# Kernel optimization log

Hardware: AMD Instinct MI355X
Metric: run time of the kernel (lower is better)

Reference implementation:

```python
import jax, jax.numpy as jnp
import numpy as np

B, S, D = 8, 512, 768
H = 12          # attention heads
E = 14          # routed experts
K = 4           # top-k experts per sequence
HID = D * 2     # expert mlp hidden (mlp_ratio=2)
SH = D * 2 * 2  # shared expert hidden (mlp_ratio * n_shared_experts)
EPS = 1e-5


def _ln(x, g, b):
    m = x.mean(-1, keepdims=True)
    v = ((x - m) ** 2).mean(-1, keepdims=True)
    return (x - m) / jnp.sqrt(v + EPS) * g + b


def _gelu(x):
    return jax.nn.gelu(x, approximate=False)


def setup_inputs() -> dict:
    key = jax.random.key(0)
    ks = jax.random.split(key, 12)
    p = lambda k, shape: jax.random.normal(k, shape, jnp.float32) * 0.02
    z = lambda *shape: jnp.zeros(shape, jnp.float32)
    return {
        "x": jax.random.normal(ks[0], (B, S, D), jnp.float32),
        "ln1_g": jnp.ones((D,), jnp.float32), "ln1_b": z(D),
        "qkv_w": p(ks[1], (D, 3 * D)),
        "proj_w": p(ks[2], (D, D)), "proj_b": z(D),
        "ln2_g": jnp.ones((D,), jnp.float32), "ln2_b": z(D),
        "router_w1": p(ks[3], (D, D)), "router_b1": z(D),
        "router_w2": p(ks[4], (D, E)), "router_b2": z(E),
        "exp_w1": p(ks[5], (E, D, HID)), "exp_b1": z(E, HID),
        "exp_w2": p(ks[6], (E, HID, D)), "exp_b2": z(E, D),
        "sh_w1": p(ks[7], (D, SH)), "sh_b1": z(SH),
        "sh_w2": p(ks[8], (SH, D)), "sh_b2": z(D),
    }


def _forward(x, ln1_g, ln1_b, qkv_w, proj_w, proj_b, ln2_g, ln2_b,
             router_w1, router_b1, router_w2, router_b2,
             exp_w1, exp_b1, exp_w2, exp_b2,
             sh_w1, sh_b1, sh_w2, sh_b2):
    dh = D // H
    scale = dh ** -0.5
    # --- attention branch ---
    h1 = _ln(x, ln1_g, ln1_b)
    qkv = (h1 @ qkv_w).reshape(B, S, 3, H, dh)
    q = jnp.moveaxis(qkv[:, :, 0], 2, 1)  # [B,H,S,dh]
    k = jnp.moveaxis(qkv[:, :, 1], 2, 1)
    v = jnp.moveaxis(qkv[:, :, 2], 2, 1)
    att = jax.nn.softmax(jnp.einsum('bhqd,bhkd->bhqk', q, k) * scale, axis=-1)
    ao = jnp.einsum('bhqk,bhkd->bqhd', att, v).reshape(B, S, D) @ proj_w + proj_b
    x2 = x + ao
    # --- MoE branch ---
    h = _ln(x2, ln2_g, ln2_b)
    seq_repr = h.mean(axis=1)                                   # [B,D]
    logits = _gelu(seq_repr @ router_w1 + router_b1) @ router_w2 + router_b2  # [B,E]
    probs = jax.nn.softmax(logits, axis=-1)
    tw, ti = jax.lax.top_k(probs, K)                            # [B,K]
    tw = jax.nn.softmax(tw, axis=-1)                            # re-normalize top-k
    w = (jax.nn.one_hot(ti, E, dtype=tw.dtype) * tw[..., None]).sum(1)  # [B,E]
    # dense all-expert compute; zero weight off the top-k replicates masked routing
    hid = _gelu(jnp.einsum('bsd,edh->ebsh', h, exp_w1) + exp_b1[:, None, None, :])
    eo = jnp.einsum('ebsh,ehd->ebsd', hid, exp_w2) + exp_b2[:, None, None, :]
    y = jnp.einsum('ebsd,be->bsd', eo, w)
    # shared experts
    y = y + _gelu(h @ sh_w1 + sh_b1) @ sh_w2 + sh_b2
    return x2 + y  # ls2 is Identity (init_values=None); aux_loss=0 in eval


def reference(x, ln1_g, ln1_b, qkv_w, proj_w, proj_b, ln2_g, ln2_b,
              router_w1, router_b1, router_w2, router_b2,
              exp_w1, exp_b1, exp_w2, exp_b2,
              sh_w1, sh_b1, sh_w2, sh_b2):
    return _forward(x, ln1_g, ln1_b, qkv_w, proj_w, proj_b, ln2_g, ln2_b,
                    router_w1, router_b1, router_w2, router_b2,
                    exp_w1, exp_b1, exp_w2, exp_b2,
                    sh_w1, sh_b1, sh_w2, sh_b2)
```

## Files before the change

### kernel.cpp

```cpp
#include <hip/hip_runtime.h>
#include <hip/hip_bf16.h>


typedef _Float16 f16x8 __attribute__((ext_vector_type(8)));
typedef float f32x4 __attribute__((ext_vector_type(4)));
typedef _Float16 f16;

__device__ __forceinline__ float gelu_fast(float x) {
  const float k2l2e = 2.f * 0.7978845608028654f * 1.4426950408889634f;
  float u = (x + 0.044715f * x * x * x) * k2l2e;
  float t = exp2f(u);
  return x * (1.f - 1.f / (t + 1.f));
}

__device__ __forceinline__ f32x4 mfma16(f16x8 a, f16x8 b, f32x4 c) {
  return __builtin_amdgcn_mfma_f32_16x16x32_f16(a, b, c, 0, 0, 0);
}

#define ASYNC_CP16(g, l)                                            \
  __builtin_amdgcn_global_load_lds(                                 \
      (const __attribute__((address_space(1))) void*)(g),           \
      (__attribute__((address_space(3))) void*)(l), 16, 0, 0)

__global__ __launch_bounds__(256) void ln_kernel(
    const float* __restrict__ x, const float* __restrict__ g,
    const float* __restrict__ bt, f16* __restrict__ out,
    float* __restrict__ mout, float* __restrict__ rout)
{
  const int row = blockIdx.x;
  const float* xr = x + (long)row * 768;
  const int t = threadIdx.x;
  float v0 = xr[t], v1 = xr[t + 256], v2 = xr[t + 512];
  __shared__ float sb[8];
  float s = v0 + v1 + v2;
  #pragma unroll
  for (int o = 32; o > 0; o >>= 1) s += __shfl_xor(s, o, 64);
  const int w = t >> 6;
  if ((t & 63) == 0) sb[w] = s;
  __syncthreads();
  const float mean = (sb[0] + sb[1] + sb[2] + sb[3]) * (1.0f / 768.0f);
  const float d0 = v0 - mean, d1 = v1 - mean, d2 = v2 - mean;
  float q = d0 * d0 + d1 * d1 + d2 * d2;
  #pragma unroll
  for (int o = 32; o > 0; o >>= 1) q += __shfl_xor(q, o, 64);
  if ((t & 63) == 0) sb[4 + w] = q;
  __syncthreads();
  const float var = (sb[4] + sb[5] + sb[6] + sb[7]) * (1.0f / 768.0f);
  const float rstd = rsqrtf(var + 1e-5f);
  f16* orow = out + (long)row * 768;
  orow[t]       = (f16)(d0 * rstd * g[t]       + bt[t]);
  orow[t + 256] = (f16)(d1 * rstd * g[t + 256] + bt[t + 256]);
  orow[t + 512] = (f16)(d2 * rstd * g[t + 512] + bt[t + 512]);
  if (t == 0) { mout[row] = mean; rout[row] = rstd; }
}

struct TransArgs {
  const float* src[6];
  f16* dst[6];
  int rows[6], cols[6];
  int start[7];
};

__global__ __launch_bounds__(256) void transpose_all(TransArgs ta) {
  const int bid = blockIdx.x;
  int m = 0;
  #pragma unroll
  for (int i = 1; i < 6; i++) if (bid >= ta.start[i]) m = i;
  const int rows = ta.rows[m], cols = ta.cols[m];
  const int tilesC = cols >> 5;
  const int perB = (rows >> 5) * tilesC;
  int local = bid - ta.start[m];
  const int z = local / perB; local -= z * perB;
  const int tr = local / tilesC, tc = local - tr * tilesC;
  const float* inb = ta.src[m] + (long)z * rows * cols;
  f16* outb = ta.dst[m] + (long)z * rows * cols;
  const int c0 = tc * 32, r0 = tr * 32;
  __shared__ float tile[32][33];
  const int tx = threadIdx.x & 31, ty = threadIdx.x >> 5;
  #pragma unroll
  for (int i = 0; i < 32; i += 8)
    tile[ty + i][tx] = inb[(long)(r0 + ty + i) * cols + c0 + tx];
  __syncthreads();
  #pragma unroll
  for (int i = 0; i < 32; i += 8)
    outb[(long)(c0 + ty + i) * rows + r0 + tx] = (f16)tile[tx][ty + i];
}

#define EPI_QKV     0
#define EPI_RESID   1
#define EPI_GELU    2
#define EPI_OUTBASE 3
#define EPI_GELUW   4
#define EPI_SCB     5

template <int EPI>
__global__ __launch_bounds__(256) void gemm_bt(
    const f16* __restrict__ A, int K, long strideA, int aShift,
    const f16* __restrict__ W, long strideW,
    const float* __restrict__ bias, int strideBias,
    const int* __restrict__ topkIdx,
    void* __restrict__ outv, long strideOut, int ldout,
    const float* __restrict__ resid)
{
  __shared__ f16 sA[128 * 32];
  __shared__ f16 sB[128 * 32];
  const int tid = threadIdx.x;
  const int pair = blockIdx.z;
  const int m0 = blockIdx.y * 128;
  const int n0 = blockIdx.x * 128;
  const f16* Ab = A + ((long)(pair >> aShift)) * strideA;
  const int wsel = topkIdx ? topkIdx[pair] : pair;
  const f16* Wb = W + (long)wsel * strideW;

  const int f = tid * 8;
  const int fr = f >> 5;
  const int fc = f & 31;
  const int lane = tid & 63, wid = tid >> 6;
  const int wm = (wid >> 1) * 64, wn = (wid & 1) * 64;
  const int lr = lane & 15, q4 = lane >> 4;

  f32x4 zero = {0.f, 0.f, 0.f, 0.f};
  f32x4 acc[4][4];
  #pragma unroll
  for (int i = 0; i < 4; i++)
    #pragma unroll
    for (int j = 0; j < 4; j++) acc[i][j] = zero;

  for (int k0 = 0; k0 < K; k0 += 32) {
    __syncthreads();
    ASYNC_CP16(&Ab[(long)(m0 + fr) * K + k0 + fc],      &sA[f]);
    ASYNC_CP16(&Ab[(long)(m0 + fr + 64) * K + k0 + fc], &sA[f + 2048]);
    ASYNC_CP16(&Wb[(long)(n0 + fr) * K + k0 + fc],      &sB[f]);
    ASYNC_CP16(&Wb[(long)(n0 + fr + 64) * K + k0 + fc], &sB[f + 2048]);
    __syncthreads();
    f16x8 av[4], bv[4];
    #pragma unroll
    for (int i = 0; i < 4; i++) av[i] = *(const f16x8*)&sA[(wm + i * 16 + lr) * 32 + q4 * 8];
    #pragma unroll
    for (int j = 0; j < 4; j++) bv[j] = *(const f16x8*)&sB[(wn + j * 16 + lr) * 32 + q4 * 8];
    #pragma unroll
    for (int i = 0; i < 4; i++)
      #pragma unroll
      for (int j = 0; j < 4; j++) acc[i][j] = mfma16(av[i], bv[j], acc[i][j]);
  }

  float wscale = 1.f;
  if constexpr (EPI == EPI_GELUW || EPI == EPI_SCB) wscale = resid[pair];

  #pragma unroll
  for (int i = 0; i < 4; i++) {
    #pragma unroll
    for (int j = 0; j < 4; j++) {
      #pragma unroll
      for (int r = 0; r < 4; r++) {
        const int row = m0 + wm + i * 16 + q4 * 4 + r;
        const int col = n0 + wn + j * 16 + lr;
        float v = acc[i][j][r];
        if constexpr (EPI == EPI_QKV) {
          f16* qb = (f16*)outv;
          const int i3 = col / 768;
          const int rem = col - i3 * 768;
          const int hh = rem >> 6, dd = rem & 63;
          const int bb = row >> 9, ss = row & 511;
          const long bh = bb * 12 + hh;
          if (i3 == 0)      qb[(bh * 512 + ss) * 64 + dd] = (f16)v;
          else if (i3 == 1) qb[3145728 + (bh * 512 + ss) * 64 + dd] = (f16)v;
          else              qb[6291456 + (bh * 64 + dd) * 512 + ss] = (f16)v;
        } else if constexpr (EPI == EPI_RESID) {
          float* ob = (float*)outv;
          v += bias[col];
          ob[(long)row * ldout + col] = resid[(long)row * ldout + col] + v;
        } else if constexpr (EPI == EPI_GELU) {
          f16* ob = (f16*)outv + (long)pair * strideOut;
          v += bias[(long)wsel * strideBias + col];
          ob[(long)row * ldout + col] = (f16)gelu_fast(v);
        } else if constexpr (EPI == EPI_OUTBASE) {
          float* ob = (float*)outv;
          v += bias[col];
          ob[(long)row * ldout + col] = resid[(long)row * ldout + col] + v;
        } else if constexpr (EPI == EPI_GELUW) {
          f16* ob = (f16*)outv + (long)pair * strideOut;
          v += bias[(long)wsel * strideBias + col];
          ob[(long)row * ldout + col] = (f16)(gelu_fast(v) * wscale);
        } else {
          f16* ob = (f16*)outv + (long)pair * strideOut;
          v += wscale * bias[(long)wsel * strideBias + col];
          ob[(long)row * ldout + col] = (f16)v;
        }
      }
    }
  }
}

__device__ __forceinline__ int pswz(int row, int col) {
  return row * 512 + (col ^ ((row & 7) << 3));
}

__global__ __launch_bounds__(256) void attn_kernel(
    const f16* __restrict__ Q, const f16* __restrict__ Kt,
    const f16* __restrict__ Vt, f16* __restrict__ AO)
{
  __shared__ f16 Ps[64 * 512];
  const int bh = blockIdx.x;
  const int qt = blockIdx.y;
  const int t = threadIdx.x;
  const int lane = t & 63, w = t >> 6;
  const int lr = lane & 15, q4 = lane >> 4;
  const int r0 = qt * 64 + w * 16;
  const int lrow0 = w * 16;
  const f16* Qh = Q + (long)bh * 512 * 64;
  const f16* Kh = Kt + (long)bh * 512 * 64;

  f32x4 zero = {0.f, 0.f, 0.f, 0.f};
  f32x4 acc[32];
  #pragma unroll
  for (int i = 0; i < 32; i++) acc[i] = zero;

  #pragma unroll
  for (int kk = 0; kk < 2; kk++) {
    f16x8 a = *(const f16x8*)&Qh[(r0 + lr) * 64 + kk * 32 + q4 * 8];
    #pragma unroll
    for (int nt = 0; nt < 32; nt++) {
      f16x8 b = *(const f16x8*)&Kh[(nt * 16 + lr) * 64 + kk * 32 + q4 * 8];
      acc[nt] = mfma16(a, b, acc[nt]);
    }
  }

  const float cscale = 0.125f * 1.44269504089f;
  #pragma unroll
  for (int r = 0; r < 4; r++) {
    float m = -1e30f;
    #pragma unroll
    for (int nt = 0; nt < 32; nt++) m = fmaxf(m, acc[nt][r]);
    #pragma unroll
    for (int o = 1; o < 16; o <<= 1) m = fmaxf(m, __shfl_xor(m, o, 64));
    float s = 0.f;
    #pragma unroll
    for (int nt = 0; nt < 32; nt++) {
      float e = exp2f((acc[nt][r] - m) * cscale);
      acc[nt][r] = e; s += e;
    }
    #pragma unroll
    for (int o = 1; o < 16; o <<= 1) s += __shfl_xor(s, o, 64);
    const float inv = 1.f / s;
    const int lrow = lrow0 + q4 * 4 + r;
    #pragma unroll
    for (int nt = 0; nt < 32; nt++)
      Ps[pswz(lrow, nt * 16 + lr)] = (f16)(acc[nt][r] * inv);
  }

  const f16* Vh = Vt + (long)bh * 64 * 512;
  f32x4 o4[4];
  #pragma unroll
  for (int i = 0; i < 4; i++) o4[i] = zero;
  #pragma unroll
  for (int kk = 0; kk < 16; kk++) {
    f16x8 a = *(const f16x8*)&Ps[pswz(lrow0 + lr, kk * 32 + q4 * 8)];
    #pragma unroll
    for (int nt = 0; nt < 4; nt++) {
      f16x8 b = *(const f16x8*)&Vh[(nt * 16 + lr) * 512 + kk * 32 + q4 * 8];
      o4[nt] = mfma16(a, b, o4[nt]);
    }
  }
  const int b_ = bh / 12, h_ = bh - b_ * 12;
  #pragma unroll
  for (int nt = 0; nt < 4; nt++)
    #pragma unroll
    for (int r = 0; r < 4; r++) {
      const int rowg = r0 + q4 * 4 + r;
      AO[((long)(b_ * 512 + rowg)) * 768 + h_ * 64 + nt * 16 + lr] = (f16)o4[nt][r];
    }
}

__global__ __launch_bounds__(256) void router_reduce(
    const float* __restrict__ x2, const float* __restrict__ lnm,
    const float* __restrict__ lnr, float* __restrict__ part)
{
  const int c = blockIdx.x, b = blockIdx.y, t = threadIdx.x;
  float a0 = 0.f, a1 = 0.f, a2 = 0.f;
  #pragma unroll 4
  for (int s = 0; s < 32; s++) {
    const long base = (long)b * 512 + c * 32 + s;
    const float m = lnm[base], r = lnr[base];
    const float* xr = x2 + base * 768;
    a0 += (xr[t] - m) * r;
    a1 += (xr[t + 256] - m) * r;
    a2 += (xr[t + 512] - m) * r;
  }
  float* pr = part + ((long)b * 16 + c) * 768;
  pr[t] = a0; pr[t + 256] = a1; pr[t + 512] = a2;
}

__global__ __launch_bounds__(256) void router_seq(
    const float* __restrict__ part, const float* __restrict__ g2,
    const float* __restrict__ b2ln, float* __restrict__ seqg)
{
  const int b = blockIdx.x, t = threadIdx.x;
  const float* pb = part + (long)b * 16 * 768;
  #pragma unroll
  for (int i = 0; i < 3; i++) {
    const int j = t + 256 * i;
    float a = 0.f;
    #pragma unroll
    for (int c = 0; c < 16; c++) a += pb[c * 768 + j];
    seqg[b * 768 + j] = a * (1.f / 512.f) * g2[j] + b2ln[j];
  }
}

__global__ __launch_bounds__(256) void router_mlp1(
    const float* __restrict__ seqg, const float* __restrict__ rw1,
    float* __restrict__ pmlp)
{
  const int c = blockIdx.x, b = blockIdx.y, t = threadIdx.x;
  const float* sq = seqg + b * 768 + c * 48;
  float a0 = 0.f, a1 = 0.f, a2 = 0.f;
  #pragma unroll 8
  for (int d = 0; d < 48; d++) {
    const float s = sq[d];
    const float* wr = rw1 + (long)(c * 48 + d) * 768;
    a0 += s * wr[t];
    a1 += s * wr[t + 256];
    a2 += s * wr[t + 512];
  }
  float* pr = pmlp + ((long)b * 16 + c) * 768;
  pr[t] = a0; pr[t + 256] = a1; pr[t + 512] = a2;
}

__global__ __launch_bounds__(256) void router_fold(
    const float* __restrict__ pmlp, const float* __restrict__ rb1,
    float* __restrict__ g1g)
{
  const int b = blockIdx.x, t = threadIdx.x;
  const float* pb = pmlp + (long)b * 16 * 768;
  #pragma unroll
  for (int i = 0; i < 3; i++) {
    const int j = t + 256 * i;
    float a = rb1[j];
    #pragma unroll
    for (int c = 0; c < 16; c++) a += pb[c * 768 + j];
    g1g[b * 768 + j] = 0.5f * a * (1.0f + erff(a * 0.70710678118654752f));
  }
}

__global__ __launch_bounds__(256) void router_top(
    const float* __restrict__ g1g, const float* __restrict__ rw2,
    const float* __restrict__ rb2, float* __restrict__ wslot,
    int* __restrict__ topkIdx)
{
  __shared__ float lg[14];
  const int b = blockIdx.x, t = threadIdx.x;
  const int e = t >> 4, sub = t & 15;
  if (e < 14) {
    float a = 0.f;
    #pragma unroll
    for (int i = 0; i < 48; i++) {
      const int d = sub + 16 * i;
      a += g1g[b * 768 + d] * rw2[d * 14 + e];
    }
    #pragma unroll
    for (int o = 1; o < 16; o <<= 1) a += __shfl_xor(a, o, 64);
    if (sub == 0) lg[e] = a + rb2[e];
  }
  __syncthreads();
  if (t == 0) {
    float mx = -1e30f;
    for (int ee = 0; ee < 14; ee++) mx = fmaxf(mx, lg[ee]);
    float p[14], s = 0.f;
    for (int ee = 0; ee < 14; ee++) { p[ee] = expf(lg[ee] - mx); s += p[ee]; }
    for (int ee = 0; ee < 14; ee++) p[ee] /= s;
    int idx[4]; float val[4]; bool used[14];
    for (int ee = 0; ee < 14; ee++) used[ee] = false;
    for (int k = 0; k < 4; k++) {
      int best = -1; float bv = -1.f;
      for (int ee = 0; ee < 14; ee++)
        if (!used[ee] && p[ee] > bv) { bv = p[ee]; best = ee; }
      used[best] = true; idx[k] = best; val[k] = bv;
    }
    const float m2 = val[0];
    float ss = 0.f, e4[4];
    for (int k = 0; k < 4; k++) { e4[k] = expf(val[k] - m2); ss += e4[k]; }
    for (int k = 0; k < 4; k++) {
      wslot[b * 4 + k] = e4[k] / ss;
      topkIdx[b * 4 + k] = idx[k];
    }
  }
}

__global__ __launch_bounds__(256) void combine_kernel(
    const f16* __restrict__ eo, float* __restrict__ out)
{
  const long i = (long)blockIdx.x * 256 + threadIdx.x;
  const long b = i / (512L * 768);
  const long loc = i - b * (512L * 768);
  const f16* e0 = eo + b * 4 * (512L * 768) + loc;
  float v = out[i];
  v += (float)e0[0] + (float)e0[512L * 768] + (float)e0[2 * 512L * 768] +
       (float)e0[3 * 512L * 768];
  out[i] = v;
}

static const long OFF_X2    = 0L;
static const long OFF_LNM   = 12582912L;
static const long OFF_LNR   = OFF_LNM + 16384L;
static const long OFF_WSLOT = OFF_LNR + 16384L;
static const long OFF_TOPK  = OFF_WSLOT + 256L;
static const long OFF_PART  = OFF_TOPK + 256L;
static const long OFF_SEQG  = OFF_PART + 393216L;
static const long OFF_PMLP  = OFF_SEQG + 24576L;
static const long OFF_G1G   = OFF_PMLP + 393216L;
static const long W_QKVWT  = 13631488L;
static const long W_PROJWT = W_QKVWT + 3538944L;
static const long W_EW1T   = W_PROJWT + 1179648L;
static const long W_EW2T   = W_EW1T + 33030144L;
static const long W_SHW1T  = W_EW2T + 33030144L;
static const long W_SHW2T  = W_SHW1T + 4718592L;
static const long OFF_ACT  = 93847552L;
static const long A_H1     = OFF_ACT;
static const long A_Q      = OFF_ACT + 6291456L;
static const long A_AO     = A_Q + 18874368L;
static const long B_H      = OFF_ACT;
static const long B_HID    = OFF_ACT + 6291456L;
static const long B_SHID   = B_HID + 50331648L;
static const long B_EO     = B_SHID;

extern "C" void kernel_launch(void* const* d_in, const int* in_sizes, int n_in,
                              void* d_out, int out_size, void* d_ws, size_t ws_size,
                              hipStream_t stream) {
  const float* x     = (const float*)d_in[0];
  const float* ln1g  = (const float*)d_in[1];
  const float* ln1b  = (const float*)d_in[2];
  const float* qkvw  = (const float*)d_in[3];
  const float* projw = (const float*)d_in[4];
  const float* projb = (const float*)d_in[5];
  const float* ln2g  = (const float*)d_in[6];
  const float* ln2b  = (const float*)d_in[7];
  const float* rw1   = (const float*)d_in[8];
  const float* rb1   = (const float*)d_in[9];
  const float* rw2   = (const float*)d_in[10];
  const float* rb2   = (const float*)d_in[11];
  const float* ew1   = (const float*)d_in[12];
  const float* eb1   = (const float*)d_in[13];
  const float* ew2   = (const float*)d_in[14];
  const float* eb2   = (const float*)d_in[15];
  const float* shw1  = (const float*)d_in[16];
  const float* shb1  = (const float*)d_in[17];
  const float* shw2  = (const float*)d_in[18];
  const float* shb2  = (const float*)d_in[19];

  char* ws = (char*)d_ws;
  float* x2    = (float*)(ws + OFF_X2);
  float* lnm   = (float*)(ws + OFF_LNM);
  float* lnr   = (float*)(ws + OFF_LNR);
  float* wslot = (float*)(ws + OFF_WSLOT);
  int*   topk  = (int*)(ws + OFF_TOPK);
  float* part  = (float*)(ws + OFF_PART);
  float* seqg  = (float*)(ws + OFF_SEQG);
  float* pmlp  = (float*)(ws + OFF_PMLP);
  float* g1g   = (float*)(ws + OFF_G1G);
  f16* qkvwt  = (f16*)(ws + W_QKVWT);
  f16* projwt = (f16*)(ws + W_PROJWT);
  f16* ew1t   = (f16*)(ws + W_EW1T);
  f16* ew2t   = (f16*)(ws + W_EW2T);
  f16* shw1t  = (f16*)(ws + W_SHW1T);
  f16* shw2t  = (f16*)(ws + W_SHW2T);
  f16* h1     = (f16*)(ws + A_H1);
  f16* Qb     = (f16*)(ws + A_Q);
  f16* aob    = (f16*)(ws + A_AO);
  f16* hbuf   = (f16*)(ws + B_H);
  f16* hid    = (f16*)(ws + B_HID);
  f16* shid   = (f16*)(ws + B_SHID);
  f16* eo     = (f16*)(ws + B_EO);

  TransArgs ta;
  ta.src[0] = qkvw;  ta.dst[0] = qkvwt;  ta.rows[0] = 768;  ta.cols[0] = 2304;
  ta.src[1] = projw; ta.dst[1] = projwt; ta.rows[1] = 768;  ta.cols[1] = 768;
  ta.src[2] = ew1;   ta.dst[2] = ew1t;   ta.rows[2] = 768;  ta.cols[2] = 1536;
  ta.src[3] = ew2;   ta.dst[3] = ew2t;   ta.rows[3] = 1536; ta.cols[3] = 768;
  ta.src[4] = shw1;  ta.dst[4] = shw1t;  ta.rows[4] = 768;  ta.cols[4] = 3072;
  ta.src[5] = shw2;  ta.dst[5] = shw2t;  ta.rows[5] = 3072; ta.cols[5] = 768;
  ta.start[0] = 0;     ta.start[1] = 1728;  ta.start[2] = 2304;
  ta.start[3] = 18432; ta.start[4] = 34560; ta.start[5] = 36864;
  ta.start[6] = 39168;
  transpose_all<<<39168, 256, 0, stream>>>(ta);

  ln_kernel<<<4096, 256, 0, stream>>>(x, ln1g, ln1b, h1, lnm, lnr);
  gemm_bt<EPI_QKV><<<dim3(18, 32, 1), 256, 0, stream>>>(
      h1, 768, 0, 0, qkvwt, 0, nullptr, 0, nullptr, (void*)Qb, 0, 0, nullptr);
  attn_kernel<<<dim3(96, 8, 1), 256, 0, stream>>>(Qb, Qb + 3145728, Qb + 6291456, aob);
  gemm_bt<EPI_RESID><<<dim3(6, 32, 1), 256, 0, stream>>>(
      aob, 768, 0, 0, projwt, 0, projb, 0, nullptr, (void*)x2, 0, 768, x);

  ln_kernel<<<4096, 256, 0, stream>>>(x2, ln2g, ln2b, hbuf, lnm, lnr);
  router_reduce<<<dim3(16, 8, 1), 256, 0, stream>>>(x2, lnm, lnr, part);
  router_seq<<<8, 256, 0, stream>>>(part, ln2g, ln2b, seqg);
  router_mlp1<<<dim3(16, 8, 1), 256, 0, stream>>>(seqg, rw1, pmlp);
  router_fold<<<8, 256, 0, stream>>>(pmlp, rb1, g1g);
  router_top<<<8, 256, 0, stream>>>(g1g, rw2, rb2, wslot, topk);
  gemm_bt<EPI_GELU><<<dim3(24, 32, 1), 256, 0, stream>>>(
      hbuf, 768, 0, 0, shw1t, 0, shb1, 0, nullptr, (void*)shid, 0, 3072, nullptr);
  gemm_bt<EPI_OUTBASE><<<dim3(6, 32, 1), 256, 0, stream>>>(
      shid, 3072, 0, 0, shw2t, 0, shb2, 0, nullptr, d_out, 0, 768, x2);
  gemm_bt<EPI_GELUW><<<dim3(12, 4, 32), 256, 0, stream>>>(
      hbuf, 768, 512L * 768, 2, ew1t, 1536L * 768, eb1, 1536, topk,
      (void*)hid, 512L * 1536, 1536, wslot);
  gemm_bt<EPI_SCB><<<dim3(6, 4, 32), 256, 0, stream>>>(
      hid, 1536, 512L * 1536, 0, ew2t, 768L * 1536, eb2, 768, topk,
      (void*)eo, 512L * 768, 768, wslot);
  combine_kernel<<<12288, 256, 0, stream>>>(eo, (float*)d_out);
}
```

Before: 666.8 us.

## Merge shared and routed expert GEMMs into combined launches with XCD-aware tiling

Replaces four separate FFN GEMM launches (shared W1, shared W2, expert W1, expert W2) with two combined kernels. Each kernel serves both the shared-expert and routed-expert tiles from one grid. Block indices are remapped so each of the 8 XCDs gets a contiguous chunk of tiles, which should improve L2 reuse. The goal is fewer launches and filling the tail of small grids. The cost is heterogeneous block work (K=3072 vs 1536 in ffn2), and eo is moved to a separate buffer so it no longer aliases shid.

```diff
diff --git a/kernel.cpp b/kernel.cpp
--- a/kernel.cpp
+++ b/kernel.cpp
@@ -21,6 +21,27 @@
   __builtin_amdgcn_global_load_lds(                                 \
       (const __attribute__((address_space(1))) void*)(g),           \
       (__attribute__((address_space(3))) void*)(l), 16, 0, 0)
+
+#define GEMM_CORE(AB, WB, KK)                                               \
+  for (int k0 = 0; k0 < (KK); k0 += 32) {                                   \
+    __syncthreads();                                                        \
+    ASYNC_CP16(&(AB)[(long)fr * (KK) + k0 + fc],        &sA[f]);            \
+    ASYNC_CP16(&(AB)[(long)(fr + 64) * (KK) + k0 + fc], &sA[f + 2048]);     \
+    ASYNC_CP16(&(WB)[(long)fr * (KK) + k0 + fc],        &sB[f]);            \
+    ASYNC_CP16(&(WB)[(long)(fr + 64) * (KK) + k0 + fc], &sB[f + 2048]);     \
+    __syncthreads();                                                        \
+    f16x8 av[4], bv[4];                                                     \
+    _Pragma("unroll")                                                       \
+    for (int i = 0; i < 4; i++)                                             \
+      av[i] = *(const f16x8*)&sA[(wm + i * 16 + lr) * 32 + q4 * 8];         \
+    _Pragma("unroll")                                                       \
+    for (int j = 0; j < 4; j++)                                             \
+      bv[j] = *(const f16x8*)&sB[(wn + j * 16 + lr) * 32 + q4 * 8];         \
+    _Pragma("unroll")                                                       \
+    for (int i = 0; i < 4; i++)                                             \
+      _Pragma("unroll")                                                     \
+      for (int j = 0; j < 4; j++) acc[i][j] = mfma16(av[i], bv[j], acc[i][j]); \
+  }
 
 __global__ __launch_bounds__(256) void ln_kernel(
     const float* __restrict__ x, const float* __restrict__ g,
@@ -88,10 +109,6 @@
 
 #define EPI_QKV     0
 #define EPI_RESID   1
-#define EPI_GELU    2
-#define EPI_OUTBASE 3
-#define EPI_GELUW   4
-#define EPI_SCB     5
 
 template <int EPI>
 __global__ __launch_bounds__(256) void gemm_bt(
@@ -108,9 +125,9 @@
   const int pair = blockIdx.z;
   const int m0 = blockIdx.y * 128;
   const int n0 = blockIdx.x * 128;
-  const f16* Ab = A + ((long)(pair >> aShift)) * strideA;
+  const f16* Ab = A + ((long)(pair >> aShift)) * strideA + (long)m0 * K;
   const int wsel = topkIdx ? topkIdx[pair] : pair;
-  const f16* Wb = W + (long)wsel * strideW;
+  const f16* Wb = W + (long)wsel * strideW + (long)n0 * K;
 
   const int f = tid * 8;
   const int fr = f >> 5;
@@ -126,26 +143,7 @@
     #pragma unroll
     for (int j = 0; j < 4; j++) acc[i][j] = zero;
 
-  for (int k0 = 0; k0 < K; k0 += 32) {
-    __syncthreads();
-    ASYNC_CP16(&Ab[(long)(m0 + fr) * K + k0 + fc],      &sA[f]);
-    ASYNC_CP16(&Ab[(long)(m0 + fr + 64) * K + k0 + fc], &sA[f + 2048]);
-    ASYNC_CP16(&Wb[(long)(n0 + fr) * K + k0 + fc],      &sB[f]);
-    ASYNC_CP16(&Wb[(long)(n0 + fr + 64) * K + k0 + fc], &sB[f + 2048]);
-    __syncthreads();
-    f16x8 av[4], bv[4];
-    #pragma unroll
-    for (int i = 0; i < 4; i++) av[i] = *(const f16x8*)&sA[(wm + i * 16 + lr) * 32 + q4 * 8];
-    #pragma unroll
-    for (int j = 0; j < 4; j++) bv[j] = *(const f16x8*)&sB[(wn + j * 16 + lr) * 32 + q4 * 8];
-    #pragma unroll
-    for (int i = 0; i < 4; i++)
-      #pragma unroll
-      for (int j = 0; j < 4; j++) acc[i][j] = mfma16(av[i], bv[j], acc[i][j]);
-  }
-
-  float wscale = 1.f;
-  if constexpr (EPI == EPI_GELUW || EPI == EPI_SCB) wscale = resid[pair];
+  GEMM_CORE(Ab, Wb, K);
 
   #pragma unroll
   for (int i = 0; i < 4; i++) {
@@ -166,29 +164,171 @@
           if (i3 == 0)      qb[(bh * 512 + ss) * 64 + dd] = (f16)v;
           else if (i3 == 1) qb[3145728 + (bh * 512 + ss) * 64 + dd] = (f16)v;
           else              qb[6291456 + (bh * 64 + dd) * 512 + ss] = (f16)v;
-        } else if constexpr (EPI == EPI_RESID) {
+        } else {
           float* ob = (float*)outv;
           v += bias[col];
           ob[(long)row * ldout + col] = resid[(long)row * ldout + col] + v;
-        } else if constexpr (EPI == EPI_GELU) {
-          f16* ob = (f16*)outv + (long)pair * strideOut;
-          v += bias[(long)wsel * strideBias + col];
-          ob[(long)row * ldout + col] = (f16)gelu_fast(v);
-        } else if constexpr (EPI == EPI_OUTBASE) {
-          float* ob = (float*)outv;
-          v += bias[col];
-          ob[(long)row * ldout + col] = resid[(long)row * ldout + col] + v;
-        } else if constexpr (EPI == EPI_GELUW) {
-          f16* ob = (f16*)outv + (long)pair * strideOut;
-          v += bias[(long)wsel * strideBias + col];
-          ob[(long)row * ldout + col] = (f16)(gelu_fast(v) * wscale);
-        } else {
-          f16* ob = (f16*)outv + (long)pair * strideOut;
-          v += wscale * bias[(long)wsel * strideBias + col];
-          ob[(long)row * ldout + col] = (f16)v;
         }
       }
     }
+  }
+}
+
+__global__ __launch_bounds__(256) void gemm_ffn1(
+    const f16* __restrict__ hbuf,
+    const f16* __restrict__ shw1t, const float* __restrict__ shb1,
+    const f16* __restrict__ ew1t,  const float* __restrict__ eb1,
+    const int* __restrict__ topk,  const float* __restrict__ wslot,
+    f16* __restrict__ shid, f16* __restrict__ hid)
+{
+  __shared__ f16 sA[128 * 32];
+  __shared__ f16 sB[128 * 32];
+  const int orig = blockIdx.x;
+  const int xcd = orig & 7, slot = orig >> 3;
+
+  const int tid = threadIdx.x;
+  const int f = tid * 8;
+  const int fr = f >> 5, fc = f & 31;
+  const int lane = tid & 63, wid = tid >> 6;
+  const int wm = (wid >> 1) * 64, wn = (wid & 1) * 64;
+  const int lr = lane & 15, q4 = lane >> 4;
+
+  const f16* Ab;
+  const f16* Wb;
+  const float* bp;
+  f16* outp;
+  int ldo;
+  float wscale;
+
+  if (slot < 96) {
+    const int l = xcd * 96 + slot;
+    const int bx = l % 24, by = l / 24;
+    const int n0 = bx * 128, m0 = by * 128;
+    Ab = hbuf + (long)m0 * 768;
+    Wb = shw1t + (long)n0 * 768;
+    bp = shb1 + n0;
+    outp = shid + (long)m0 * 3072 + n0;
+    ldo = 3072;
+    wscale = 1.f;
+  } else {
+    const int l = xcd * 192 + (slot - 96);
+    const int bx = l % 12;
+    const int u = l / 12;
+    const int by = u & 3, pair = u >> 2;
+    const int wsel = topk[pair];
+    const int n0 = bx * 128;
+    const int m0g = (pair >> 2) * 512 + by * 128;
+    Ab = hbuf + (long)m0g * 768;
+    Wb = ew1t + (long)wsel * (1536L * 768) + (long)n0 * 768;
+    bp = eb1 + (long)wsel * 1536 + n0;
+    outp = hid + (long)pair * (512L * 1536) + (long)(by * 128) * 1536 + n0;
+    ldo = 1536;
+    wscale = wslot[pair];
+  }
+
+  f32x4 zero = {0.f, 0.f, 0.f, 0.f};
+  f32x4 acc[4][4];
+  #pragma unroll
+  for (int i = 0; i < 4; i++)
+    #pragma unroll
+    for (int j = 0; j < 4; j++) acc[i][j] = zero;
+
+  GEMM_CORE(Ab, Wb, 768);
+
+  #pragma unroll
+  for (int i = 0; i < 4; i++)
+    #pragma unroll
+    for (int j = 0; j < 4; j++)
+      #pragma unroll
+      for (int r = 0; r < 4; r++) {
+        const int rr = wm + i * 16 + q4 * 4 + r;
+        const int cc = wn + j * 16 + lr;
+        float v = acc[i][j][r] + bp[cc];
+        outp[(long)rr * ldo + cc] = (f16)(gelu_fast(v) * wscale);
+      }
+}
+
+__global__ __launch_bounds__(256) void gemm_ffn2(
+    const f16* __restrict__ shid, const f16* __restrict__ shw2t,
+    const float* __restrict__ shb2, const float* __restrict__ x2,
+    const f16* __restrict__ hid, const f16* __restrict__ ew2t,
+    const float* __restrict__ eb2,
+    const int* __restrict__ topk, const float* __restrict__ wslot,
+    float* __restrict__ dout, f16* __restrict__ eo)
+{
+  __shared__ f16 sA[128 * 32];
+  __shared__ f16 sB[128 * 32];
+  const int orig = blockIdx.x;
+  const int xcd = orig & 7, slot = orig >> 3;
+
+  const int tid = threadIdx.x;
+  const int f = tid * 8;
+  const int fr = f >> 5, fc = f & 31;
+  const int lane = tid & 63, wid = tid >> 6;
+  const int wm = (wid >> 1) * 64, wn = (wid & 1) * 64;
+  const int lr = lane & 15, q4 = lane >> 4;
+
+  const bool shared_role = (slot < 24);
+  const f16* Ab;
+  const f16* Wb;
+  int K, m0, n0, pair = 0, wsel = 0;
+
+  if (shared_role) {
+    const int l = xcd * 24 + slot;
+    const int bx = l % 6, by = l / 6;
+    n0 = bx * 128; m0 = by * 128;
+    K = 3072;
+    Ab = shid + (long)m0 * 3072;
+    Wb = shw2t + (long)n0 * 3072;
+  } else {
+    const int l = xcd * 96 + (slot - 24);
+    const int bx = l % 6;
+    const int u = l / 6;
+    const int by = u & 3; pair = u >> 2;
+    wsel = topk[pair];
+    n0 = bx * 128; m0 = by * 128;
+    K = 1536;
+    Ab = hid + (long)pair * (512L * 1536) + (long)m0 * 1536;
+    Wb = ew2t + (long)wsel * (768L * 1536) + (long)n0 * 1536;
+  }
+
+  f32x4 zero = {0.f, 0.f, 0.f, 0.f};
+  f32x4 acc[4][4];
+  #pragma unroll
+  for (int i = 0; i < 4; i++)
+    #pragma unroll
+    for (int j = 0; j < 4; j++) acc[i][j] = zero;
+
+  GEMM_CORE(Ab, Wb, K);
+
+  if (shared_role) {
+    float* op = dout + (long)m0 * 768 + n0;
+    const float* rp = x2 + (long)m0 * 768 + n0;
+    const float* bp = shb2 + n0;
+    #pragma unroll
+    for (int i = 0; i < 4; i++)
+      #pragma unroll
+      for (int j = 0; j < 4; j++)
+        #pragma unroll
+        for (int r = 0; r < 4; r++) {
+          const int rr = wm + i * 16 + q4 * 4 + r;
+          const int cc = wn + j * 16 + lr;
+          op[(long)rr * 768 + cc] = rp[(long)rr * 768 + cc] + acc[i][j][r] + bp[cc];
+        }
+  } else {
+    const float wscale = wslot[pair];
+    f16* op = eo + (long)pair * (512L * 768) + (long)m0 * 768 + n0;
+    const float* bp = eb2 + (long)wsel * 768 + n0;
+    #pragma unroll
+    for (int i = 0; i < 4; i++)
+      #pragma unroll
+      for (int j = 0; j < 4; j++)
+        #pragma unroll
+        for (int r = 0; r < 4; r++) {
+          const int rr = wm + i * 16 + q4 * 4 + r;
+          const int cc = wn + j * 16 + lr;
+          op[(long)rr * 768 + cc] = (f16)(acc[i][j][r] + wscale * bp[cc]);
+        }
   }
 }
 
@@ -421,7 +561,7 @@
 static const long B_H      = OFF_ACT;
 static const long B_HID    = OFF_ACT + 6291456L;
 static const long B_SHID   = B_HID + 50331648L;
-static const long B_EO     = B_SHID;
+static const long B_EO     = B_SHID + 25165824L;
 
 extern "C" void kernel_launch(void* const* d_in, const int* in_sizes, int n_in,
                               void* d_out, int out_size, void* d_ws, size_t ws_size,
@@ -496,15 +636,9 @@
   router_mlp1<<<dim3(16, 8, 1), 256, 0, stream>>>(seqg, rw1, pmlp);
   router_fold<<<8, 256, 0, stream>>>(pmlp, rb1, g1g);
   router_top<<<8, 256, 0, stream>>>(g1g, rw2, rb2, wslot, topk);
-  gemm_bt<EPI_GELU><<<dim3(24, 32, 1), 256, 0, stream>>>(
-      hbuf, 768, 0, 0, shw1t, 0, shb1, 0, nullptr, (void*)shid, 0, 3072, nullptr);
-  gemm_bt<EPI_OUTBASE><<<dim3(6, 32, 1), 256, 0, stream>>>(
-      shid, 3072, 0, 0, shw2t, 0, shb2, 0, nullptr, d_out, 0, 768, x2);
-  gemm_bt<EPI_GELUW><<<dim3(12, 4, 32), 256, 0, stream>>>(
-      hbuf, 768, 512L * 768, 2, ew1t, 1536L * 768, eb1, 1536, topk,
-      (void*)hid, 512L * 1536, 1536, wslot);
-  gemm_bt<EPI_SCB><<<dim3(6, 4, 32), 256, 0, stream>>>(
-      hid, 1536, 512L * 1536, 0, ew2t, 768L * 1536, eb2, 768, topk,
-      (void*)eo, 512L * 768, 768, wslot);
+  gemm_ffn1<<<2304, 256, 0, stream>>>(hbuf, shw1t, shb1, ew1t, eb1,
+                                      topk, wslot, shid, hid);
+  gemm_ffn2<<<960, 256, 0, stream>>>(shid, shw2t, shb2, x2, hid, ew2t, eb2,
+                                     topk, wslot, (float*)d_out, eo);
   combine_kernel<<<12288, 256, 0, stream>>>(eo, (float*)d_out);
 }
```

After: 600.8 us. -9.9%, faster.
